# Kernel tuning notes

Hardware: AMD Instinct MI355X
Metric: run time of the kernel (lower is better)

Reference implementation:

```python
import jax, jax.numpy as jnp
import numpy as np

B, S, D, H, F = 16, 512, 768, 12, 3072
E = 4      # unique sequence-level experts
M = 4      # inner SwitchFeedForward experts
SW = 128   # switch encoder dim
EPS = 1e-12


def setup_inputs() -> dict:
    key = jax.random.key(0)
    ks = iter(jax.random.split(key, 64))
    def p(shape):
        return jax.random.normal(next(ks), shape, jnp.float32) * 0.02
    inp = {}
    inp['hidden_states'] = jax.random.normal(next(ks), (B, S, D), jnp.float32)
    inp['attention_mask'] = jnp.zeros((B, S), jnp.float32)
    inp['cluster_list'] = jnp.zeros((B,), jnp.int32)
    # router
    inp['sw_enc_w'] = p((D, SW)); inp['sw_enc_b'] = jnp.zeros((SW,), jnp.float32)
    inp['sw_w'] = p((SW, E));     inp['sw_b'] = jnp.zeros((E,), jnp.float32)
    # common attention
    for n in ('q', 'k', 'v', 'o'):
        inp['ca_w' + n] = p((D, D)); inp['ca_b' + n] = jnp.zeros((D,), jnp.float32)
    # unique attentions (stacked over E experts)
    for n in ('q', 'k', 'v', 'o'):
        inp['ua_w' + n] = p((E, D, D)); inp['ua_b' + n] = jnp.zeros((E, D), jnp.float32)
    # common FFN (plain GELU MLP)
    inp['cf_w1'] = p((D, F)); inp['cf_b1'] = jnp.zeros((F,), jnp.float32)
    inp['cf_w2'] = p((F, D)); inp['cf_b2'] = jnp.zeros((D,), jnp.float32)
    # unique FFNs: each is a top-1 SwitchFeedForward with M inner experts
    inp['uf_sw_w'] = p((E, D, M)); inp['uf_sw_b'] = jnp.zeros((E, M), jnp.float32)
    inp['uf_w1'] = p((E, M, D, F)); inp['uf_b1'] = jnp.zeros((E, M, F), jnp.float32)
    inp['uf_w2'] = p((E, M, F, D)); inp['uf_b2'] = jnp.zeros((E, M, D), jnp.float32)
    # output LayerNorm
    inp['ln_g'] = jnp.ones((D,), jnp.float32); inp['ln_b'] = jnp.zeros((D,), jnp.float32)
    return inp


def _attn(x, mask, wq, bq, wk, bk, wv, bv, wo, bo):
    b, s, d = x.shape
    dh = d // H
    q = (x @ wq + bq).reshape(b, s, H, dh)
    k = (x @ wk + bk).reshape(b, s, H, dh)
    v = (x @ wv + bv).reshape(b, s, H, dh)
    sc = jnp.einsum('bqhd,bkhd->bhqk', q, k) / jnp.sqrt(jnp.float32(dh))
    sc = sc + mask[:, None, None, :]
    pr = jax.nn.softmax(sc, axis=-1)
    o = jnp.einsum('bhqk,bkhd->bqhd', pr, v).reshape(b, s, d)
    return o @ wo + bo


def _switch_ffn(x, sww, swb, w1, b1, w2, b2):
    # top-1 token routing over M inner experts, output scaled by route_prob_max
    rp = jax.nn.softmax(x @ sww + swb, axis=-1)            # [b,s,M]
    gate = jax.nn.one_hot(jnp.argmax(rp, -1), M) * jnp.max(rp, -1, keepdims=True)
    h = jax.nn.gelu(jnp.einsum('bsd,mdf->bsmf', x, w1) + b1, approximate=False)
    y = jnp.einsum('bsmf,mfd->bsmd', h, w2) + b2
    return jnp.einsum('bsm,bsmd->bsd', gate, y)


def _forward(hidden_states, attention_mask, sw_enc_w, sw_enc_b, sw_w, sw_b,
             ca_wq, ca_bq, ca_wk, ca_bk, ca_wv, ca_bv, ca_wo, ca_bo,
             ua_wq, ua_bq, ua_wk, ua_bk, ua_wv, ua_bv, ua_wo, ua_bo,
             cf_w1, cf_b1, cf_w2, cf_b2,
             uf_sw_w, uf_sw_b, uf_w1, uf_b1, uf_w2, uf_b2, ln_g, ln_b):
    # sequence-level router: softmax over pooled hidden states, top-1 expert
    pooled = hidden_states.mean(axis=1)                    # [B,D]
    rp = jax.nn.softmax((pooled @ sw_enc_w + sw_enc_b) @ sw_w + sw_b, axis=-1)
    pm = jnp.max(rp, axis=-1)                              # [B]
    sel = jax.nn.one_hot(jnp.argmax(rp, axis=-1), E)       # [B,E]

    common_attn = _attn(hidden_states, attention_mask,
                        ca_wq, ca_bq, ca_wk, ca_bk, ca_wv, ca_bv, ca_wo, ca_bo)
    unique_attn = jnp.zeros_like(hidden_states)
    for i in range(E):
        oi = _attn(hidden_states, attention_mask,
                   ua_wq[i], ua_bq[i], ua_wk[i], ua_bk[i],
                   ua_wv[i], ua_bv[i], ua_wo[i], ua_bo[i])
        unique_attn = unique_attn + sel[:, i, None, None] * oi
    unique_attn = unique_attn * pm[:, None, None]          # scale by route prob
    att_output = common_attn + unique_attn

    unique_ffn = jnp.zeros_like(hidden_states)
    for i in range(E):
        yi = _switch_ffn(att_output, uf_sw_w[i], uf_sw_b[i],
                         uf_w1[i], uf_b1[i], uf_w2[i], uf_b2[i])
        unique_ffn = unique_ffn + sel[:, i, None, None] * yi
    common_ffn = jax.nn.gelu(att_output @ cf_w1 + cf_b1, approximate=False) @ cf_w2 + cf_b2
    ffn_output = common_ffn + unique_ffn                   # dropout is identity (eval)

    x = att_output + ffn_output
    mu = x.mean(-1, keepdims=True)
    var = jnp.mean((x - mu) ** 2, -1, keepdims=True)
    return (x - mu) / jnp.sqrt(var + EPS) * ln_g + ln_b


def reference(hidden_states, attention_mask, cluster_list, sw_enc_w, sw_enc_b, sw_w, sw_b,
              ca_wq, ca_bq, ca_wk, ca_bk, ca_wv, ca_bv, ca_wo, ca_bo,
              ua_wq, ua_bq, ua_wk, ua_bk, ua_wv, ua_bv, ua_wo, ua_bo,
              cf_w1, cf_b1, cf_w2, cf_b2,
              uf_sw_w, uf_sw_b, uf_w1, uf_b1, uf_w2, uf_b2, ln_g, ln_b):
    # cluster_list is only used in the warm-up branch; warm_up_step=0 -> ignored
    return _forward(hidden_states, attention_mask, sw_enc_w, sw_enc_b, sw_w, sw_b,
                    ca_wq, ca_bq, ca_wk, ca_bk, ca_wv, ca_bv, ca_wo, ca_bo,
                    ua_wq, ua_bq, ua_wk, ua_bk, ua_wv, ua_bv, ua_wo, ua_bo,
                    cf_w1, cf_b1, cf_w2, cf_b2,
                    uf_sw_w, uf_sw_b, uf_w1, uf_b1, uf_w2, uf_b2, ln_g, ln_b)
```

## Files before the change

kernel.cpp:

```cpp
#include <hip/hip_runtime.h>
#include <cstdint>
#include <cstddef>

#define Bq  16
#define Sq  512
#define Dq  768
#define Hq  12
#define DHq 64
#define Fq  3072
#define SWq 128
#define NTq 8192

typedef float        f32x4  __attribute__((ext_vector_type(4)));
typedef float        f32x16 __attribute__((ext_vector_type(16)));
typedef unsigned int u32x4  __attribute__((ext_vector_type(4)));
typedef __bf16       bf16x8 __attribute__((ext_vector_type(8)));
typedef _Float16     f16x8  __attribute__((ext_vector_type(8)));
typedef _Float16     f16x4  __attribute__((ext_vector_type(4)));
typedef _Float16     f16x2  __attribute__((ext_vector_type(2)));
typedef int          i32x2  __attribute__((ext_vector_type(2)));

__device__ __forceinline__ unsigned short f2bf(float f){
  unsigned int u = __builtin_bit_cast(unsigned int, f);
  u = (u + 0x7fffu + ((u >> 16) & 1u)) >> 16;
  return (unsigned short)u;
}
__device__ __forceinline__ unsigned int pk2(float a, float b){
  return (unsigned int)f2bf(a) | ((unsigned int)f2bf(b) << 16);
}
__device__ __forceinline__ i32x2 pl32swap(unsigned int a, unsigned int b){
  return __builtin_amdgcn_permlane32_swap((int)a, (int)b, false, false);
}
__device__ __forceinline__ f16x2 cvt_pk(float a, float b){
  return __builtin_bit_cast(f16x2, __builtin_amdgcn_cvt_pkrtz(a, b));
}

typedef __attribute__((address_space(1))) void vg_t;
typedef __attribute__((address_space(3))) void vl_t;
__device__ __forceinline__ void gl_lds16(const void* g, void* l){
  __builtin_amdgcn_global_load_lds((vg_t*)g, (vl_t*)l, 16, 0, 0);
}

__device__ __forceinline__ void swz2d(int &bx, int &by){
  const int gx = gridDim.x, gy = gridDim.y;
  const int nb = gx * gy;
  const int bid = blockIdx.y * gx + blockIdx.x;
  if (((nb & 7) == 0) && ((gy & 7) == 0)){
    const int chunk = nb >> 3;
    const int lb = (bid & 7) * chunk + (bid >> 3);
    const int bw = gx << 3;
    const int band = lb / bw;
    const int wn = lb - band * bw;
    bx = wn >> 3;
    by = (band << 3) + (wn & 7);
  } else {
    bx = blockIdx.x; by = blockIdx.y;
  }
}

__global__ void pooled_partial_k(const float* __restrict__ x, float* __restrict__ part){
  const int b = blockIdx.x, dc = blockIdx.y, z = blockIdx.z;
  const int d = dc*256 + threadIdx.x;
  const float* p = x + (size_t)b*Sq*Dq + (size_t)z*128*Dq + d;
  float s = 0.f;
  #pragma unroll 4
  for (int i = 0; i < 128; i++) s += p[(size_t)i*Dq];
  part[((size_t)z*Bq + b)*Dq + d] = s;
}

__global__ void router_seq_k(const float* __restrict__ part,
    const float* __restrict__ ew, const float* __restrict__ eb,
    const float* __restrict__ sw, const float* __restrict__ sb,
    int* __restrict__ sel, float* __restrict__ pm)
{
  const int b = blockIdx.x, j = threadIdx.x;
  __shared__ float h[SWq];
  __shared__ float pl[Dq];
  #pragma unroll
  for (int i = 0; i < 6; i++){
    int d = j + i*128;
    float s = part[(size_t)(0*Bq+b)*Dq + d] + part[(size_t)(1*Bq+b)*Dq + d]
            + part[(size_t)(2*Bq+b)*Dq + d] + part[(size_t)(3*Bq+b)*Dq + d];
    pl[d] = s * (1.0f/512.0f);
  }
  __syncthreads();
  float a = eb[j];
  for (int d = 0; d < Dq; d++) a += pl[d] * ew[d*SWq + j];
  h[j] = a;
  __syncthreads();
  if (j == 0){
    float lg[4];
    for (int e = 0; e < 4; e++){
      float t = sb[e];
      for (int k = 0; k < SWq; k++) t += h[k] * sw[k*4 + e];
      lg[e] = t;
    }
    float mx = fmaxf(fmaxf(lg[0],lg[1]), fmaxf(lg[2],lg[3]));
    float p[4], ssum = 0.f;
    for (int e = 0; e < 4; e++){ p[e] = expf(lg[e]-mx); ssum += p[e]; }
    int am = 0; float bv = p[0];
    for (int e = 1; e < 4; e++) if (p[e] > bv){ bv = p[e]; am = e; }
    sel[b] = am; pm[b] = bv/ssum;
  }
}

__global__ void split_f16_k(const float* __restrict__ x, _Float16* __restrict__ hh,
                            _Float16* __restrict__ ll, int n4){
  const int i = blockIdx.x*256 + threadIdx.x;
  if (i >= n4) return;
  f32x4 v = ((const f32x4*)x)[i];
  f16x4 vh, vl;
  #pragma unroll
  for (int j = 0; j < 4; j++){
    float s = v[j] * 1024.0f;
    _Float16 a = (_Float16)s;
    vh[j] = a;
    vl[j] = (_Float16)(s - (float)a);
  }
  ((f16x4*)hh)[i] = vh;
  ((f16x4*)ll)[i] = vl;
}

__global__ void transpose_f16s_k(const float* __restrict__ src,
    _Float16* __restrict__ dH, _Float16* __restrict__ dL,
    int K, int N, long srcStride, long dstStride, int rowOff)
{
  __shared__ float t[64][65];
  const int tid = threadIdx.x;
  const size_t so = (size_t)blockIdx.z * srcStride;
  const size_t dof = (size_t)blockIdx.z * dstStride;
  const int k0 = blockIdx.y * 64, n0 = blockIdx.x * 64;
  const int r = tid >> 2, c0 = (tid & 3) * 16;
  const float* sp = src + so + (size_t)(k0 + r) * N + n0 + c0;
  #pragma unroll
  for (int cc = 0; cc < 16; cc += 4){
    f32x4 v = *(const f32x4*)(sp + cc);
    t[r][c0+cc] = v[0]; t[r][c0+cc+1] = v[1]; t[r][c0+cc+2] = v[2]; t[r][c0+cc+3] = v[3];
  }
  __syncthreads();
  _Float16* ph = dH + dof + (size_t)(rowOff + n0 + r) * K + k0 + c0;
  _Float16* pl = dL + dof + (size_t)(rowOff + n0 + r) * K + k0 + c0;
  #pragma unroll
  for (int cc = 0; cc < 16; cc += 4){
    f16x4 vh, vl;
    #pragma unroll
    for (int j = 0; j < 4; j++){
      float s = t[c0+cc+j][r] * 1024.0f;
      _Float16 a = (_Float16)s;
      vh[j] = a; vl[j] = (_Float16)(s - (float)a);
    }
    *(f16x4*)(ph + cc) = vh;
    *(f16x4*)(pl + cc) = vl;
  }
}

__global__ void concat_bias3_k(const float* __restrict__ bq, const float* __restrict__ bk,
    const float* __restrict__ bv, float* __restrict__ dst, int srcStride)
{
  const int e = blockIdx.y;
  const int i = blockIdx.x*256 + threadIdx.x;
  dst[(size_t)e*2304 + i]        = bq[(size_t)e*srcStride + i];
  dst[(size_t)e*2304 + 768 + i]  = bk[(size_t)e*srcStride + i];
  dst[(size_t)e*2304 + 1536 + i] = bv[(size_t)e*srcStride + i];
}

template<int MT, int BMODE, int OMODE>
__global__ __launch_bounds__(256,2) void gemm_f16s_k(
    const _Float16* __restrict__ AH, const _Float16* __restrict__ AL,
    const _Float16* __restrict__ BH, const _Float16* __restrict__ BL,
    const float* __restrict__ bias, float* __restrict__ C,
    _Float16* __restrict__ Ch, _Float16* __restrict__ Cl,
    int N, int K, long estride, int bias_stride,
    const int* __restrict__ sel, const float* __restrict__ pm)
{
  constexpr int MI = MT / 32;
  constexpr int AI = MT / 64;
  __shared__ _Float16 AsH[MT][32];
  __shared__ _Float16 AsL[MT][32];
  __shared__ _Float16 BsH[128][32];
  __shared__ _Float16 BsL[128][32];
  const int tid = threadIdx.x;
  const int lane = tid & 63, wave = tid >> 6;
  const int wm = wave >> 1, wn = wave & 1;
  int bx, by; swz2d(bx, by);
  const int row0 = by * MT, col0 = bx * 128;
  const _Float16* bh = BH; const _Float16* bl = BL; const float* bp = bias;
  float cs = 1.0f;
  if constexpr (BMODE == 1){
    const int e = sel[row0 >> 9];
    bh += (size_t)e * estride; bl += (size_t)e * estride;
    bp += (size_t)e * bias_stride;
  }
  if constexpr (OMODE == 1) cs = pm[row0 >> 9];

  const int lr = lane >> 2, lk = (lane & 3) * 8;
  const _Float16 *pAH[AI], *pAL[AI], *pBH[2], *pBL[2];
  _Float16 *lAH[AI], *lAL[AI], *lBH[2], *lBL[2];
  #pragma unroll
  for (int j = 0; j < AI; j++){
    const int ia = wave*AI + j;
    pAH[j] = AH + (size_t)(row0 + ia*16 + lr)*K + lk;
    pAL[j] = AL + (size_t)(row0 + ia*16 + lr)*K + lk;
    lAH[j] = &AsH[0][0] + ia*512;
    lAL[j] = &AsL[0][0] + ia*512;
  }
  #pragma unroll
  for (int j = 0; j < 2; j++){
    const int ib = wave*2 + j;
    pBH[j] = bh + (size_t)(col0 + ib*16 + lr)*K + lk;
    pBL[j] = bl + (size_t)(col0 + ib*16 + lr)*K + lk;
    lBH[j] = &BsH[0][0] + ib*512;
    lBL[j] = &BsL[0][0] + ib*512;
  }

  f32x4 acc[MI][4];
  #pragma unroll
  for (int mi=0;mi<MI;mi++)
    #pragma unroll
    for (int ni=0;ni<4;ni++) acc[mi][ni] = (f32x4){0.f,0.f,0.f,0.f};

  for (int k0 = 0; k0 < K; k0 += 32){
    __syncthreads();
    #pragma unroll
    for (int j = 0; j < AI; j++){
      gl_lds16(pAH[j] + k0, lAH[j]);
      gl_lds16(pAL[j] + k0, lAL[j]);
    }
    #pragma unroll
    for (int j = 0; j < 2; j++){
      gl_lds16(pBH[j] + k0, lBH[j]);
      gl_lds16(pBL[j] + k0, lBL[j]);
    }
    __syncthreads();
    f16x8 fah[MI], fal[MI], fbh[4], fbl[4];
    #pragma unroll
    for (int mi=0;mi<MI;mi++){
      const int r = wm*(MT/2) + mi*16 + (lane&15), c = 8*(lane>>4);
      fah[mi] = __builtin_bit_cast(f16x8, *(const u32x4*)&AsH[r][c]);
      fal[mi] = __builtin_bit_cast(f16x8, *(const u32x4*)&AsL[r][c]);
    }
    #pragma unroll
    for (int ni=0;ni<4;ni++){
      const int r = wn*64 + ni*16 + (lane&15), c = 8*(lane>>4);
      fbh[ni] = __builtin_bit_cast(f16x8, *(const u32x4*)&BsH[r][c]);
      fbl[ni] = __builtin_bit_cast(f16x8, *(const u32x4*)&BsL[r][c]);
    }
    #pragma unroll
    for (int mi=0;mi<MI;mi++)
      #pragma unroll
      for (int ni=0;ni<4;ni++){
        acc[mi][ni] = __builtin_amdgcn_mfma_f32_16x16x32_f16(fah[mi], fbh[ni], acc[mi][ni], 0, 0, 0);
        acc[mi][ni] = __builtin_amdgcn_mfma_f32_16x16x32_f16(fah[mi], fbl[ni], acc[mi][ni], 0, 0, 0);
        acc[mi][ni] = __builtin_amdgcn_mfma_f32_16x16x32_f16(fal[mi], fbh[ni], acc[mi][ni], 0, 0, 0);
      }
  }

  const float INV = 1.0f/1048576.0f;
  const int erow = 4*(lane >> 4);
  const int ecol = lane & 15;
  #pragma unroll
  for (int mi=0;mi<MI;mi++)
    #pragma unroll
    for (int ni=0;ni<4;ni++){
      const int c = col0 + wn*64 + ni*16 + ecol;
      const float bb = bp[c];
      #pragma unroll
      for (int r=0;r<4;r++){
        const int R = row0 + wm*(MT/2) + mi*16 + erow + r;
        const float v = acc[mi][ni][r]*INV + bb;
        if constexpr (OMODE == 0){
          C[(size_t)R*N + c] = v;
        } else if constexpr (OMODE == 1){
          C[(size_t)R*N + c] += cs*v;
        } else {
          const float vs = v * 1024.0f;
          const _Float16 hi = (_Float16)vs;
          Ch[(size_t)R*N + c] = hi;
          Cl[(size_t)R*N + c] = (_Float16)(vs - (float)hi);
        }
      }
    }
}

__global__ __launch_bounds__(256,2) void attn_mfma_k(
    const _Float16* __restrict__ qkvH, const _Float16* __restrict__ qkvL,
    const float* __restrict__ mask,
    _Float16* __restrict__ ctxH, _Float16* __restrict__ ctxL)
{
  __shared__ _Float16 Kh[64][72], Kl[64][72];
  __shared__ _Float16 Vh[64][72], Vl[64][72];
  __shared__ float msk[64];
  __shared__ float rsi[4][32];
  const int qb = blockIdx.x, h = blockIdx.y, b = blockIdx.z;
  const int tid = threadIdx.x;
  const int l = tid & 63, w = tid >> 6;
  const int l31 = l & 31, g5 = l >> 5;
  const float SC = 1.0f/8388608.0f;

  u32x4 qfh[4], qfl[4];
  {
    const size_t qoff = (size_t)(b*Sq + qb*128 + w*32 + l31) * 2304 + h*DHq + g5*8;
    #pragma unroll
    for (int c = 0; c < 4; c++){
      qfh[c] = *(const u32x4*)(qkvH + qoff + c*16);
      qfl[c] = *(const u32x4*)(qkvL + qoff + c*16);
    }
  }
  f32x16 oacc[2];
  #pragma unroll
  for (int nt = 0; nt < 2; nt++)
    #pragma unroll
    for (int i = 0; i < 16; i++) oacc[nt][i] = 0.f;
  float rsl = 0.f;
  const float* mrow = mask + b*Sq;

  for (int kt = 0; kt < 8; kt++){
    __syncthreads();
    {
      const size_t krow = (size_t)(b*Sq + kt*64 + l) * 2304 + 768 + h*DHq;
      #pragma unroll
      for (int i = 0; i < 2; i++){
        const int ch = w + i*4;
        *(u32x4*)&Kh[l][ch*8] = *(const u32x4*)(qkvH + krow + ch*8);
        *(u32x4*)&Kl[l][ch*8] = *(const u32x4*)(qkvL + krow + ch*8);
      }
      const size_t vrow = krow + 768 + w*16;
      f16x8 v0 = __builtin_bit_cast(f16x8, *(const u32x4*)(qkvH + vrow));
      f16x8 v1 = __builtin_bit_cast(f16x8, *(const u32x4*)(qkvH + vrow + 8));
      f16x8 u0 = __builtin_bit_cast(f16x8, *(const u32x4*)(qkvL + vrow));
      f16x8 u1 = __builtin_bit_cast(f16x8, *(const u32x4*)(qkvL + vrow + 8));
      #pragma unroll
      for (int i = 0; i < 8; i++){
        Vh[w*16 + i][l] = v0[i]; Vh[w*16 + 8 + i][l] = v1[i];
        Vl[w*16 + i][l] = u0[i]; Vl[w*16 + 8 + i][l] = u1[i];
      }
      if (tid < 64) msk[tid] = mrow[kt*64 + tid] + 6.9314718055994531f;
    }
    __syncthreads();

    f32x16 sacc[2];
    #pragma unroll
    for (int mt = 0; mt < 2; mt++)
      #pragma unroll
      for (int i = 0; i < 16; i++) sacc[mt][i] = 0.f;
    #pragma unroll
    for (int mt = 0; mt < 2; mt++){
      #pragma unroll
      for (int c = 0; c < 4; c++){
        f16x8 kh = __builtin_bit_cast(f16x8, *(const u32x4*)&Kh[mt*32 + l31][c*16 + g5*8]);
        f16x8 kl = __builtin_bit_cast(f16x8, *(const u32x4*)&Kl[mt*32 + l31][c*16 + g5*8]);
        f16x8 qh = __builtin_bit_cast(f16x8, qfh[c]);
        f16x8 ql = __builtin_bit_cast(f16x8, qfl[c]);
        sacc[mt] = __builtin_amdgcn_mfma_f32_32x32x16_f16(kh, qh, sacc[mt], 0, 0, 0);
        sacc[mt] = __builtin_amdgcn_mfma_f32_32x32x16_f16(kh, ql, sacc[mt], 0, 0, 0);
        sacc[mt] = __builtin_amdgcn_mfma_f32_32x32x16_f16(kl, qh, sacc[mt], 0, 0, 0);
      }
    }

    unsigned int hP[2][4][2], lP[2][4][2];
    #pragma unroll
    for (int mt = 0; mt < 2; mt++){
      #pragma unroll
      for (int m = 0; m < 4; m++){
        f32x4 mk = *(const f32x4*)&msk[mt*32 + m*8 + g5*4];
        float p0 = __expf(fmaf(sacc[mt][4*m+0], SC, mk[0]));
        float p1 = __expf(fmaf(sacc[mt][4*m+1], SC, mk[1]));
        float p2 = __expf(fmaf(sacc[mt][4*m+2], SC, mk[2]));
        float p3 = __expf(fmaf(sacc[mt][4*m+3], SC, mk[3]));
        rsl += (p0 + p1) + (p2 + p3);
        f16x2 h0 = cvt_pk(p0, p1);
        f16x2 h1 = cvt_pk(p2, p3);
        f16x2 e0, e1;
        e0[0] = (_Float16)(p0 - (float)h0[0]); e0[1] = (_Float16)(p1 - (float)h0[1]);
        e1[0] = (_Float16)(p2 - (float)h1[0]); e1[1] = (_Float16)(p3 - (float)h1[1]);
        hP[mt][m][0] = __builtin_bit_cast(unsigned int, h0);
        hP[mt][m][1] = __builtin_bit_cast(unsigned int, h1);
        lP[mt][m][0] = __builtin_bit_cast(unsigned int, e0);
        lP[mt][m][1] = __builtin_bit_cast(unsigned int, e1);
      }
    }

    #pragma unroll
    for (int mt = 0; mt < 2; mt++){
      #pragma unroll
      for (int cc = 0; cc < 2; cc++){
        i32x2 sh0 = pl32swap(hP[mt][2*cc][0], hP[mt][2*cc+1][0]);
        i32x2 sh1 = pl32swap(hP[mt][2*cc][1], hP[mt][2*cc+1][1]);
        i32x2 sl0 = pl32swap(lP[mt][2*cc][0], lP[mt][2*cc+1][0]);
        i32x2 sl1 = pl32swap(lP[mt][2*cc][1], lP[mt][2*cc+1][1]);
        u32x4 pah = (u32x4){(unsigned)sh0[0], (unsigned)sh1[0], (unsigned)sh0[1], (unsigned)sh1[1]};
        u32x4 pal = (u32x4){(unsigned)sl0[0], (unsigned)sl1[0], (unsigned)sl0[1], (unsigned)sl1[1]};
        f16x8 ph = __builtin_bit_cast(f16x8, pah);
        f16x8 pe = __builtin_bit_cast(f16x8, pal);
        const int kof = (mt*2 + cc)*16 + g5*8;
        #pragma unroll
        for (int nt = 0; nt < 2; nt++){
          f16x8 vh = __builtin_bit_cast(f16x8, *(const u32x4*)&Vh[nt*32 + l31][kof]);
          f16x8 vl = __builtin_bit_cast(f16x8, *(const u32x4*)&Vl[nt*32 + l31][kof]);
          oacc[nt] = __builtin_amdgcn_mfma_f32_32x32x16_f16(ph, vh, oacc[nt], 0, 0, 0);
          oacc[nt] = __builtin_amdgcn_mfma_f32_32x32x16_f16(ph, vl, oacc[nt], 0, 0, 0);
          oacc[nt] = __builtin_amdgcn_mfma_f32_32x32x16_f16(pe, vh, oacc[nt], 0, 0, 0);
        }
      }
    }
  }

  {
    unsigned int rb = __builtin_bit_cast(unsigned int, rsl);
    i32x2 sw = pl32swap(rb, rb);
    float partner = __builtin_bit_cast(float, (l >= 32) ? sw[0] : sw[1]);
    float tot = rsl + partner;
    if (l < 32) rsi[w][l31] = 1.0f / tot;
  }
  __syncthreads();

  const size_t obase = (size_t)(b*Sq + qb*128 + w*32);
  #pragma unroll
  for (int nt = 0; nt < 2; nt++){
    const int col = h*DHq + nt*32 + l31;
    #pragma unroll
    for (int r = 0; r < 16; r++){
      const int q = (r&3) + 8*(r>>2) + 4*g5;
      const float v = oacc[nt][r] * rsi[w][q];
      const _Float16 hi = (_Float16)v;
      const size_t off = (obase + q)*Dq + col;
      ctxH[off] = hi;
      ctxL[off] = (_Float16)(v - (float)hi);
    }
  }
}

__global__ void transpose_bf16_k(const float* __restrict__ src, unsigned short* __restrict__ dst,
                                 int K, int N)
{
  __shared__ float t[64][65];
  const int tid = threadIdx.x;
  const size_t mo = (size_t)blockIdx.z * K * N;
  const int k0 = blockIdx.y * 64, n0 = blockIdx.x * 64;
  const int r = tid >> 2, c0 = (tid & 3) * 16;
  const float* sp = src + mo + (size_t)(k0 + r) * N + n0 + c0;
  #pragma unroll
  for (int cc = 0; cc < 16; cc += 4){
    f32x4 v = *(const f32x4*)(sp + cc);
    t[r][c0+cc] = v[0]; t[r][c0+cc+1] = v[1]; t[r][c0+cc+2] = v[2]; t[r][c0+cc+3] = v[3];
  }
  __syncthreads();
  unsigned short* dp = dst + mo + (size_t)(n0 + r) * K + k0 + c0;
  u32x4 h0, h1v;
  #pragma unroll
  for (int i = 0; i < 4; i++) h0[i]  = pk2(t[c0+2*i  ][r], t[c0+2*i+1][r]);
  #pragma unroll
  for (int i = 0; i < 4; i++) h1v[i] = pk2(t[c0+8+2*i][r], t[c0+9+2*i][r]);
  *(u32x4*)(dp)     = h0;
  *(u32x4*)(dp + 8) = h1v;
}

template<int MT, int AMODE, int OMODE, bool GELU_, bool GROUPED>
__global__ __launch_bounds__(256,2) void gemm_bf16_k(
    const void* __restrict__ Av, const unsigned short* __restrict__ BT,
    const float* __restrict__ bias, float* __restrict__ Cf, unsigned short* __restrict__ Cb,
    int N, int K,
    const int* __restrict__ tile_g, const int* __restrict__ tile_r0,
    const int* __restrict__ grp_off, const int* __restrict__ n_tiles,
    const int* __restrict__ tok_idx, const float* __restrict__ gate_s,
    size_t bstride, int bias_stride)
{
  constexpr int MI = MT / 32;
  constexpr int AI = MT / 64;
  __shared__ unsigned short As[2][MT][32];
  __shared__ unsigned short Bs[2][128][32];
  const int tid = threadIdx.x;
  const int lane = tid & 63, wave = tid >> 6;
  const int wm = wave >> 1, wn = wave & 1;
  int col0, row0, gend = 1 << 30, g = 0;
  if constexpr (GROUPED){
    const int gx = gridDim.x;
    const int nb = gx * gridDim.y;
    const int bid = blockIdx.y * gx + blockIdx.x;
    int lb = bid;
    if ((nb & 7) == 0) lb = (bid & 7) * (nb >> 3) + (bid >> 3);
    const int t = lb / gx;
    col0 = (lb - t * gx) * 128;
    if (t >= *n_tiles) return;
    g = tile_g[t];
    row0 = grp_off[g] + tile_r0[t];
    gend = grp_off[g+1];
  } else {
    int bx, by; swz2d(bx, by);
    row0 = by * MT;
    col0 = bx * 128;
  }
  const unsigned short* Bp = BT + (size_t)g * bstride;
  const float* bp = bias + (size_t)g * bias_stride;

  const int lr = lane >> 2, lk8 = (lane & 3) * 8;
  const unsigned short* pB[2];
  #pragma unroll
  for (int j = 0; j < 2; j++){
    const int ib = wave*2 + j;
    pB[j] = Bp + (size_t)(col0 + ib*16 + lr)*K + lk8;
  }
  auto stageB = [&](int c, int kk){
    gl_lds16(pB[0] + kk, &Bs[0][0][0] + c*4096 + (wave*2+0)*512);
    gl_lds16(pB[1] + kk, &Bs[0][0][0] + c*4096 + (wave*2+1)*512);
  };
  const unsigned short* pA2[AI];
  const float* afp = nullptr; int sa_r = 0, sa_k = 0;
  if constexpr (AMODE == 2){
    #pragma unroll
    for (int j = 0; j < AI; j++){
      int r = row0 + (wave*AI + j)*16 + lr;
      if constexpr (GROUPED) r = (r < gend - 1) ? r : (gend - 1);
      pA2[j] = (const unsigned short*)Av + (size_t)r*K + lk8;
    }
  } else {
    sa_r = (MT == 128) ? (tid >> 1) : (tid >> 2);
    sa_k = (MT == 128) ? ((tid & 1) * 16) : ((tid & 3) * 8);
    int arow = row0 + sa_r;
    if constexpr (GROUPED) arow = (arow < gend - 1) ? arow : (gend - 1);
    if constexpr (AMODE == 1) arow = tok_idx[arow];
    afp = (const float*)Av + (size_t)arow * K + sa_k;
  }
  auto stageA2 = [&](int c, int kk){
    #pragma unroll
    for (int j = 0; j < AI; j++)
      gl_lds16(pA2[j] + kk, &As[0][0][0] + c*(MT*32) + (wave*AI + j)*512);
  };

  f32x4 acc[MI][4];
  #pragma unroll
  for (int mi=0;mi<MI;mi++)
    #pragma unroll
    for (int ni=0;ni<4;ni++) acc[mi][ni] = (f32x4){0.f,0.f,0.f,0.f};

  const int nt = K >> 5;
  if constexpr (AMODE == 2){
    stageA2(0, 0);
  } else {
    f32x4 f0 = *(const f32x4*)(afp);
    f32x4 f1 = *(const f32x4*)(afp + 4);
    u32x4 al0;
    al0[0]=pk2(f0[0],f0[1]); al0[1]=pk2(f0[2],f0[3]); al0[2]=pk2(f1[0],f1[1]); al0[3]=pk2(f1[2],f1[3]);
    *(u32x4*)&As[0][sa_r][sa_k] = al0;
    if constexpr (MT == 128){
      f32x4 f2 = *(const f32x4*)(afp + 8);
      f32x4 f3 = *(const f32x4*)(afp + 12);
      u32x4 al1;
      al1[0]=pk2(f2[0],f2[1]); al1[1]=pk2(f2[2],f2[3]); al1[2]=pk2(f3[0],f3[1]); al1[3]=pk2(f3[2],f3[3]);
      *(u32x4*)&As[0][sa_r][sa_k + 8] = al1;
    }
  }
  stageB(0, 0);

  int cur = 0;
  for (int t = 0; t < nt; t++){
    __syncthreads();
    const int k1 = (t + 1) << 5;
    f32x4 f0n, f1n, f2n, f3n;
    const bool nxt = (t + 1 < nt);
    if (nxt){
      if constexpr (AMODE == 2){
        stageA2(cur ^ 1, k1);
      } else {
        f0n = *(const f32x4*)(afp + k1);
        f1n = *(const f32x4*)(afp + k1 + 4);
        if constexpr (MT == 128){
          f2n = *(const f32x4*)(afp + k1 + 8);
          f3n = *(const f32x4*)(afp + k1 + 12);
        }
      }
      stageB(cur ^ 1, k1);
    }
    bf16x8 af[MI], bfr[4];
    #pragma unroll
    for (int mi=0;mi<MI;mi++){
      u32x4 tt = *(const u32x4*)&As[cur][wm*(MT/2) + mi*16 + (lane&15)][8*(lane>>4)];
      af[mi] = __builtin_bit_cast(bf16x8, tt);
    }
    #pragma unroll
    for (int ni=0;ni<4;ni++){
      u32x4 tt = *(const u32x4*)&Bs[cur][wn*64 + ni*16 + (lane&15)][8*(lane>>4)];
      bfr[ni] = __builtin_bit_cast(bf16x8, tt);
    }
    #pragma unroll
    for (int mi=0;mi<MI;mi++)
      #pragma unroll
      for (int ni=0;ni<4;ni++)
        acc[mi][ni] = __builtin_amdgcn_mfma_f32_16x16x32_bf16(af[mi], bfr[ni], acc[mi][ni], 0, 0, 0);
    if (nxt){
      if constexpr (AMODE != 2){
        u32x4 al0;
        al0[0]=pk2(f0n[0],f0n[1]); al0[1]=pk2(f0n[2],f0n[3]); al0[2]=pk2(f1n[0],f1n[1]); al0[3]=pk2(f1n[2],f1n[3]);
        *(u32x4*)&As[cur^1][sa_r][sa_k] = al0;
        if constexpr (MT == 128){
          u32x4 al1;
          al1[0]=pk2(f2n[0],f2n[1]); al1[1]=pk2(f2n[2],f2n[3]); al1[2]=pk2(f3n[0],f3n[1]); al1[3]=pk2(f3n[2],f3n[3]);
          *(u32x4*)&As[cur^1][sa_r][sa_k + 8] = al1;
        }
      }
    }
    cur ^= 1;
  }

  const int erow = 4*(lane >> 4);
  const int ecol = lane & 15;
  #pragma unroll
  for (int mi=0;mi<MI;mi++)
    #pragma unroll
    for (int ni=0;ni<4;ni++){
      const int c = col0 + wn*64 + ni*16 + ecol;
      const float bb = bp[c];
      #pragma unroll
      for (int r=0;r<4;r++){
        const int R = row0 + wm*(MT/2) + mi*16 + erow + r;
        if (GROUPED && R >= gend) continue;
        float v = acc[mi][ni][r] + bb;
        if (GELU_) v = 0.5f*v*(1.0f + erff(v*0.70710678118654752f));
        if constexpr (OMODE == 0){
          Cb[(size_t)R*N + c] = f2bf(v);
        } else if constexpr (OMODE == 1){
          Cf[(size_t)R*N + c] = v;
        } else {
          const int tok = tok_idx[R];
          const float gt = gate_s[R];
          float* p = Cf + (size_t)tok*N + c;
          *p += gt*v;
        }
      }
    }
}

__global__ void token_router_k(const float* __restrict__ att, const int* __restrict__ sel,
    const float* __restrict__ sww, const float* __restrict__ swb,
    int* __restrict__ grp, float* __restrict__ gate, int* __restrict__ grp_cnt)
{
  const int t = blockIdx.x*4 + (threadIdx.x >> 6);
  const int lane = threadIdx.x & 63;
  const int e = sel[t >> 9];
  const float* x = att + (size_t)t * Dq;
  const float* w = sww + (size_t)e * Dq * 4;
  float a0=0.f, a1=0.f, a2=0.f, a3=0.f;
  #pragma unroll 4
  for (int i = 0; i < 12; i++){
    const int d = lane + i*64;
    const float xv = x[d];
    f32x4 wv = *(const f32x4*)&w[d*4];
    a0 += xv*wv[0]; a1 += xv*wv[1]; a2 += xv*wv[2]; a3 += xv*wv[3];
  }
  #pragma unroll
  for (int off = 32; off; off >>= 1){
    a0 += __shfl_xor(a0, off); a1 += __shfl_xor(a1, off);
    a2 += __shfl_xor(a2, off); a3 += __shfl_xor(a3, off);
  }
  if (lane == 0){
    const float l0 = a0 + swb[e*4+0], l1 = a1 + swb[e*4+1];
    const float l2 = a2 + swb[e*4+2], l3 = a3 + swb[e*4+3];
    const float mx = fmaxf(fmaxf(l0,l1), fmaxf(l2,l3));
    const float p0 = expf(l0-mx), p1 = expf(l1-mx), p2 = expf(l2-mx), p3 = expf(l3-mx);
    const float ssum = p0+p1+p2+p3;
    int am = 0; float bv = p0;
    if (p1 > bv){ bv=p1; am=1; }
    if (p2 > bv){ bv=p2; am=2; }
    if (p3 > bv){ bv=p3; am=3; }
    grp[t] = e*4 + am;
    gate[t] = bv/ssum;
    atomicAdd(&grp_cnt[e*4 + am], 1);
  }
}

__global__ void build_offsets_k(const int* __restrict__ grp_cnt, int* __restrict__ grp_off,
    int* __restrict__ tg128, int* __restrict__ tr128, int* __restrict__ nt128,
    int* __restrict__ tg64, int* __restrict__ tr64, int* __restrict__ nt64)
{
  int off = 0, n1 = 0, n2 = 0;
  for (int g = 0; g < 16; g++){
    grp_off[g] = off;
    const int c = grp_cnt[g];
    for (int r0 = 0; r0 < c; r0 += 128){ tg128[n1] = g; tr128[n1] = r0; n1++; }
    for (int r0 = 0; r0 < c; r0 += 64){  tg64[n2]  = g; tr64[n2]  = r0; n2++; }
    off += c;
  }
  grp_off[16] = off;
  *nt128 = n1; *nt64 = n2;
}

__global__ void scatter_k(const int* __restrict__ grp, const float* __restrict__ gate,
    const int* __restrict__ grp_off, int* __restrict__ fill,
    int* __restrict__ tok_idx, float* __restrict__ gate_s)
{
  const int t = blockIdx.x*256 + threadIdx.x;
  const int g = grp[t];
  const int pos = grp_off[g] + atomicAdd(&fill[g], 1);
  tok_idx[pos] = t;
  gate_s[pos] = gate[t];
}

__global__ __launch_bounds__(256) void final_ln_k(const float* __restrict__ att,
    const float* __restrict__ acc, const float* __restrict__ lg,
    const float* __restrict__ lb, float* __restrict__ out)
{
  const int row = blockIdx.x, tid = threadIdx.x;
  const float* a = att + (size_t)row * Dq;
  const float* c = acc + (size_t)row * Dq;
  float x[3];
  #pragma unroll
  for (int i = 0; i < 3; i++) x[i] = a[tid + 256*i] + c[tid + 256*i];
  __shared__ float red[256];
  red[tid] = x[0] + x[1] + x[2];
  __syncthreads();
  for (int st = 128; st; st >>= 1){
    if (tid < st) red[tid] += red[tid + st];
    __syncthreads();
  }
  const float mu = red[0] * (1.0f/768.0f);
  __syncthreads();
  const float d0 = x[0]-mu, d1 = x[1]-mu, d2 = x[2]-mu;
  red[tid] = d0*d0 + d1*d1 + d2*d2;
  __syncthreads();
  for (int st = 128; st; st >>= 1){
    if (tid < st) red[tid] += red[tid + st];
    __syncthreads();
  }
  const float inv = 1.0f/sqrtf(red[0]*(1.0f/768.0f) + 1e-12f);
  #pragma unroll
  for (int i = 0; i < 3; i++){
    const int col = tid + 256*i;
    out[(size_t)row*Dq + col] = (x[i]-mu)*inv*lg[col] + lb[col];
  }
}

extern "C" void kernel_launch(void* const* d_in, const int* in_sizes, int n_in,
                              void* d_out, int out_size, void* d_ws, size_t ws_size,
                              hipStream_t stream)
{
  (void)in_sizes; (void)n_in; (void)out_size; (void)ws_size;
  const float* hs    = (const float*)d_in[0];
  const float* amask = (const float*)d_in[1];
  const float* sw_enc_w = (const float*)d_in[3];
  const float* sw_enc_b = (const float*)d_in[4];
  const float* sw_w  = (const float*)d_in[5];
  const float* sw_b  = (const float*)d_in[6];
  const float* ca_wq = (const float*)d_in[7];
  const float* ca_bq = (const float*)d_in[8];
  const float* ca_wk = (const float*)d_in[9];
  const float* ca_bk = (const float*)d_in[10];
  const float* ca_wv = (const float*)d_in[11];
  const float* ca_bv = (const float*)d_in[12];
  const float* ca_wo = (const float*)d_in[13];
  const float* ca_bo = (const float*)d_in[14];
  const float* ua_wq = (const float*)d_in[15];
  const float* ua_bq = (const float*)d_in[16];
  const float* ua_wk = (const float*)d_in[17];
  const float* ua_bk = (const float*)d_in[18];
  const float* ua_wv = (const float*)d_in[19];
  const float* ua_bv = (const float*)d_in[20];
  const float* ua_wo = (const float*)d_in[21];
  const float* ua_bo = (const float*)d_in[22];
  const float* cf_w1 = (const float*)d_in[23];
  const float* cf_b1 = (const float*)d_in[24];
  const float* cf_w2 = (const float*)d_in[25];
  const float* cf_b2 = (const float*)d_in[26];
  const float* uf_sw_w = (const float*)d_in[27];
  const float* uf_sw_b = (const float*)d_in[28];
  const float* uf_w1 = (const float*)d_in[29];
  const float* uf_b1 = (const float*)d_in[30];
  const float* uf_w2 = (const float*)d_in[31];
  const float* uf_b2 = (const float*)d_in[32];
  const float* ln_g  = (const float*)d_in[33];
  const float* ln_b  = (const float*)d_in[34];
  float* out = (float*)d_out;

  char* W = (char*)d_ws;
  int*   sel     = (int*)(W + 0);
  float* pm      = (float*)(W + 64);
  int*   grp_cnt = (int*)(W + 128);
  int*   fill    = (int*)(W + 192);
  int*   ntile   = (int*)(W + 256);
  int*   ntile64 = (int*)(W + 320);
  int*   grp_off = (int*)(W + 512);
  int*   tile_g  = (int*)(W + 1024);
  int*   tile_r  = (int*)(W + 2048);
  int*   tile_g64= (int*)(W + 3072);
  int*   tile_r64= (int*)(W + 4096);

  float* att  = (float*)(W + 8192);
  float* facc = (float*)(W + 25174016);
  const size_t X = 50339840;
  _Float16* hsH  = (_Float16*)(W + X);
  _Float16* hsL  = (_Float16*)(W + X + 12582912);
  _Float16* qkvH = (_Float16*)(W + X + 25165824);
  _Float16* qkvL = (_Float16*)(W + X + 62914560);
  _Float16* ctxH = (_Float16*)(W + X + 100663296);
  _Float16* ctxL = (_Float16*)(W + X + 113246208);
  _Float16* wqkv_cH = (_Float16*)(W + X + 125829120);
  _Float16* wqkv_cL = (_Float16*)(W + X + 129368064);
  _Float16* wqkv_uH = (_Float16*)(W + X + 132907008);
  _Float16* wqkv_uL = (_Float16*)(W + X + 147062784);
  _Float16* wo_cH   = (_Float16*)(W + X + 161218560);
  _Float16* wo_cL   = (_Float16*)(W + X + 162398208);
  _Float16* wo_uH   = (_Float16*)(W + X + 163577856);
  _Float16* wo_uL   = (_Float16*)(W + X + 168296448);
  float* qkvb_c = (float*)(W + X + 173015040);
  float* qkvb_u = (float*)(W + X + 173024256);
  float* partb  = (float*)(W + X + 173061120);

  unsigned short* w1T = (unsigned short*)(W + X);
  unsigned short* w2T = (unsigned short*)(W + X + 80216064);
  unsigned short* h1  = (unsigned short*)(W + X + 160432128);
  int*   grp     = (int*)(W + 261103616);
  float* gate    = (float*)(W + 261136384);
  int*   tok_idx = (int*)(W + 261169152);
  float* gate_s  = (float*)(W + 261201920);

  hipMemsetAsync(W, 0, 512, stream);

  pooled_partial_k<<<dim3(Bq,3,4),256,0,stream>>>(hs, partb);
  router_seq_k<<<Bq,128,0,stream>>>(partb, sw_enc_w, sw_enc_b, sw_w, sw_b, sel, pm);

  split_f16_k<<<6144,256,0,stream>>>(hs, hsH, hsL, NTq*Dq/4);
  transpose_f16s_k<<<dim3(12,12,1),256,0,stream>>>(ca_wq, wqkv_cH, wqkv_cL, Dq, Dq, 0, 0, 0);
  transpose_f16s_k<<<dim3(12,12,1),256,0,stream>>>(ca_wk, wqkv_cH, wqkv_cL, Dq, Dq, 0, 0, 768);
  transpose_f16s_k<<<dim3(12,12,1),256,0,stream>>>(ca_wv, wqkv_cH, wqkv_cL, Dq, Dq, 0, 0, 1536);
  transpose_f16s_k<<<dim3(12,12,4),256,0,stream>>>(ua_wq, wqkv_uH, wqkv_uL, Dq, Dq, (long)Dq*Dq, (long)2304*768, 0);
  transpose_f16s_k<<<dim3(12,12,4),256,0,stream>>>(ua_wk, wqkv_uH, wqkv_uL, Dq, Dq, (long)Dq*Dq, (long)2304*768, 768);
  transpose_f16s_k<<<dim3(12,12,4),256,0,stream>>>(ua_wv, wqkv_uH, wqkv_uL, Dq, Dq, (long)Dq*Dq, (long)2304*768, 1536);
  transpose_f16s_k<<<dim3(12,12,1),256,0,stream>>>(ca_wo, wo_cH, wo_cL, Dq, Dq, 0, 0, 0);
  transpose_f16s_k<<<dim3(12,12,4),256,0,stream>>>(ua_wo, wo_uH, wo_uL, Dq, Dq, (long)Dq*Dq, (long)Dq*Dq, 0);
  concat_bias3_k<<<dim3(3,1),256,0,stream>>>(ca_bq, ca_bk, ca_bv, qkvb_c, 0);
  concat_bias3_k<<<dim3(3,4),256,0,stream>>>(ua_bq, ua_bk, ua_bv, qkvb_u, 768);

  gemm_f16s_k<128,0,2><<<dim3(18,64),256,0,stream>>>(hsH, hsL, wqkv_cH, wqkv_cL, qkvb_c,
      nullptr, qkvH, qkvL, 2304, Dq, 0, 0, nullptr, nullptr);
  attn_mfma_k<<<dim3(4,Hq,Bq),256,0,stream>>>(qkvH, qkvL, amask, ctxH, ctxL);
  gemm_f16s_k<64,0,0><<<dim3(6,128),256,0,stream>>>(ctxH, ctxL, wo_cH, wo_cL, ca_bo,
      att, nullptr, nullptr, Dq, Dq, 0, 0, nullptr, nullptr);

  gemm_f16s_k<128,1,2><<<dim3(18,64),256,0,stream>>>(hsH, hsL, wqkv_uH, wqkv_uL, qkvb_u,
      nullptr, qkvH, qkvL, 2304, Dq, (long)2304*768, 2304, sel, nullptr);
  attn_mfma_k<<<dim3(4,Hq,Bq),256,0,stream>>>(qkvH, qkvL, amask, ctxH, ctxL);
  gemm_f16s_k<64,1,1><<<dim3(6,128),256,0,stream>>>(ctxH, ctxL, wo_uH, wo_uL, ua_bo,
      att, nullptr, nullptr, Dq, Dq, (long)Dq*Dq, Dq, sel, pm);

  transpose_bf16_k<<<dim3(48,12,1), 256,0,stream>>>(cf_w1, w1T, Dq, Fq);
  transpose_bf16_k<<<dim3(48,12,16),256,0,stream>>>(uf_w1, w1T + 2359296, Dq, Fq);
  transpose_bf16_k<<<dim3(12,48,1), 256,0,stream>>>(cf_w2, w2T, Fq, Dq);
  transpose_bf16_k<<<dim3(12,48,16),256,0,stream>>>(uf_w2, w2T + 2359296, Fq, Dq);

  gemm_bf16_k<128,0,0,true,false><<<dim3(24,64),256,0,stream>>>((const void*)att, w1T, cf_b1, nullptr, h1,
      Fq, Dq, nullptr,nullptr,nullptr,nullptr,nullptr,nullptr, (size_t)0, 0);
  gemm_bf16_k<64,2,1,false,false><<<dim3(6,128),256,0,stream>>>((const void*)h1, w2T, cf_b2, facc, nullptr,
      Dq, Fq, nullptr,nullptr,nullptr,nullptr,nullptr,nullptr, (size_t)0, 0);

  token_router_k<<<2048,256,0,stream>>>(att, sel, uf_sw_w, uf_sw_b, grp, gate, grp_cnt);
  build_offsets_k<<<1,1,0,stream>>>(grp_cnt, grp_off, tile_g, tile_r, ntile, tile_g64, tile_r64, ntile64);
  scatter_k<<<32,256,0,stream>>>(grp, gate, grp_off, fill, tok_idx, gate_s);

  gemm_bf16_k<128,1,0,true,true><<<dim3(24,80),256,0,stream>>>((const void*)att, w1T + 2359296, uf_b1, nullptr, h1,
      Fq, Dq, tile_g, tile_r, grp_off, ntile, tok_idx, gate_s, (size_t)2359296, Fq);
  gemm_bf16_k<64,2,2,false,true><<<dim3(6,144),256,0,stream>>>((const void*)h1, w2T + 2359296, uf_b2, facc, nullptr,
      Dq, Fq, tile_g64, tile_r64, grp_off, ntile64, tok_idx, gate_s, (size_t)2359296, Dq);

  final_ln_k<<<NTq,256,0,stream>>>(att, facc, ln_g, ln_b, out);
}
```

Baseline: 1.148 ms.

## Emit bf16 copy of attention output in epilogue and accumulate FFN into att

The attention output-projection GEMMs now also write a bf16 copy of the attention output, so the FFN GEMMs load A through direct global-to-LDS async copies instead of converting fp32 to bf16 in registers. The FFN down-projections accumulate straight into the attention buffer, which removes the separate facc buffer and one read in the final LayerNorm. Token routing is moved earlier, before the transposes, but still reads fp32 att before the common FFN adds into it. The cost is an extra bf16 write in the attention epilogue, and the OMODE 1 path becomes a read-modify-write, so results depend on kernel ordering.

Measured after the change: 1.133 ms. About the same (-1.4%).

```diff
diff --git a/kernel.cpp b/kernel.cpp
--- a/kernel.cpp
+++ b/kernel.cpp
@@ -170,6 +170,7 @@
     const _Float16* __restrict__ BH, const _Float16* __restrict__ BL,
     const float* __restrict__ bias, float* __restrict__ C,
     _Float16* __restrict__ Ch, _Float16* __restrict__ Cl,
+    unsigned short* __restrict__ Cb16,
     int N, int K, long estride, int bias_stride,
     const int* __restrict__ sel, const float* __restrict__ pm)
 {
@@ -270,8 +271,11 @@
         const float v = acc[mi][ni][r]*INV + bb;
         if constexpr (OMODE == 0){
           C[(size_t)R*N + c] = v;
+          Cb16[(size_t)R*N + c] = f2bf(v);
         } else if constexpr (OMODE == 1){
-          C[(size_t)R*N + c] += cs*v;
+          const float val = C[(size_t)R*N + c] + cs*v;
+          C[(size_t)R*N + c] = val;
+          Cb16[(size_t)R*N + c] = f2bf(val);
         } else {
           const float vs = v * 1024.0f;
           const _Float16 hi = (_Float16)vs;
@@ -455,9 +459,9 @@
   *(u32x4*)(dp + 8) = h1v;
 }
 
-template<int MT, int AMODE, int OMODE, bool GELU_, bool GROUPED>
+template<int MT, bool GATHER, int OMODE, bool GELU_, bool GROUPED>
 __global__ __launch_bounds__(256,2) void gemm_bf16_k(
-    const void* __restrict__ Av, const unsigned short* __restrict__ BT,
+    const unsigned short* __restrict__ A, const unsigned short* __restrict__ BT,
     const float* __restrict__ bias, float* __restrict__ Cf, unsigned short* __restrict__ Cb,
     int N, int K,
     const int* __restrict__ tile_g, const int* __restrict__ tile_r0,
@@ -504,27 +508,18 @@
     gl_lds16(pB[0] + kk, &Bs[0][0][0] + c*4096 + (wave*2+0)*512);
     gl_lds16(pB[1] + kk, &Bs[0][0][0] + c*4096 + (wave*2+1)*512);
   };
-  const unsigned short* pA2[AI];
-  const float* afp = nullptr; int sa_r = 0, sa_k = 0;
-  if constexpr (AMODE == 2){
-    #pragma unroll
-    for (int j = 0; j < AI; j++){
-      int r = row0 + (wave*AI + j)*16 + lr;
-      if constexpr (GROUPED) r = (r < gend - 1) ? r : (gend - 1);
-      pA2[j] = (const unsigned short*)Av + (size_t)r*K + lk8;
-    }
-  } else {
-    sa_r = (MT == 128) ? (tid >> 1) : (tid >> 2);
-    sa_k = (MT == 128) ? ((tid & 1) * 16) : ((tid & 3) * 8);
-    int arow = row0 + sa_r;
-    if constexpr (GROUPED) arow = (arow < gend - 1) ? arow : (gend - 1);
-    if constexpr (AMODE == 1) arow = tok_idx[arow];
-    afp = (const float*)Av + (size_t)arow * K + sa_k;
-  }
-  auto stageA2 = [&](int c, int kk){
+  const unsigned short* pA[AI];
+  #pragma unroll
+  for (int j = 0; j < AI; j++){
+    int r = row0 + (wave*AI + j)*16 + lr;
+    if constexpr (GROUPED) r = (r < gend - 1) ? r : (gend - 1);
+    if constexpr (GATHER) r = tok_idx[r];
+    pA[j] = A + (size_t)r*K + lk8;
+  }
+  auto stageA = [&](int c, int kk){
     #pragma unroll
     for (int j = 0; j < AI; j++)
-      gl_lds16(pA2[j] + kk, &As[0][0][0] + c*(MT*32) + (wave*AI + j)*512);
+      gl_lds16(pA[j] + kk, &As[0][0][0] + c*(MT*32) + (wave*AI + j)*512);
   };
 
   f32x4 acc[MI][4];
@@ -534,41 +529,15 @@
     for (int ni=0;ni<4;ni++) acc[mi][ni] = (f32x4){0.f,0.f,0.f,0.f};
 
   const int nt = K >> 5;
-  if constexpr (AMODE == 2){
-    stageA2(0, 0);
-  } else {
-    f32x4 f0 = *(const f32x4*)(afp);
-    f32x4 f1 = *(const f32x4*)(afp + 4);
-    u32x4 al0;
-    al0[0]=pk2(f0[0],f0[1]); al0[1]=pk2(f0[2],f0[3]); al0[2]=pk2(f1[0],f1[1]); al0[3]=pk2(f1[2],f1[3]);
-    *(u32x4*)&As[0][sa_r][sa_k] = al0;
-    if constexpr (MT == 128){
-      f32x4 f2 = *(const f32x4*)(afp + 8);
-      f32x4 f3 = *(const f32x4*)(afp + 12);
-      u32x4 al1;
-      al1[0]=pk2(f2[0],f2[1]); al1[1]=pk2(f2[2],f2[3]); al1[2]=pk2(f3[0],f3[1]); al1[3]=pk2(f3[2],f3[3]);
-      *(u32x4*)&As[0][sa_r][sa_k + 8] = al1;
-    }
-  }
+  stageA(0, 0);
   stageB(0, 0);
 
   int cur = 0;
   for (int t = 0; t < nt; t++){
     __syncthreads();
     const int k1 = (t + 1) << 5;
-    f32x4 f0n, f1n, f2n, f3n;
-    const bool nxt = (t + 1 < nt);
-    if (nxt){
-      if constexpr (AMODE == 2){
-        stageA2(cur ^ 1, k1);
-      } else {
-        f0n = *(const f32x4*)(afp + k1);
-        f1n = *(const f32x4*)(afp + k1 + 4);
-        if constexpr (MT == 128){
-          f2n = *(const f32x4*)(afp + k1 + 8);
-          f3n = *(const f32x4*)(afp + k1 + 12);
-        }
-      }
+    if (t + 1 < nt){
+      stageA(cur ^ 1, k1);
       stageB(cur ^ 1, k1);
     }
     bf16x8 af[MI], bfr[4];
@@ -587,18 +556,6 @@
       #pragma unroll
       for (int ni=0;ni<4;ni++)
         acc[mi][ni] = __builtin_amdgcn_mfma_f32_16x16x32_bf16(af[mi], bfr[ni], acc[mi][ni], 0, 0, 0);
-    if (nxt){
-      if constexpr (AMODE != 2){
-        u32x4 al0;
-        al0[0]=pk2(f0n[0],f0n[1]); al0[1]=pk2(f0n[2],f0n[3]); al0[2]=pk2(f1n[0],f1n[1]); al0[3]=pk2(f1n[2],f1n[3]);
-        *(u32x4*)&As[cur^1][sa_r][sa_k] = al0;
-        if constexpr (MT == 128){
-          u32x4 al1;
-          al1[0]=pk2(f2n[0],f2n[1]); al1[1]=pk2(f2n[2],f2n[3]); al1[2]=pk2(f3n[0],f3n[1]); al1[3]=pk2(f3n[2],f3n[3]);
-          *(u32x4*)&As[cur^1][sa_r][sa_k + 8] = al1;
-        }
-      }
-    }
     cur ^= 1;
   }
 
@@ -619,7 +576,7 @@
         if constexpr (OMODE == 0){
           Cb[(size_t)R*N + c] = f2bf(v);
         } else if constexpr (OMODE == 1){
-          Cf[(size_t)R*N + c] = v;
+          Cf[(size_t)R*N + c] += v;
         } else {
           const int tok = tok_idx[R];
           const float gt = gate_s[R];
@@ -696,15 +653,13 @@
 }
 
 __global__ __launch_bounds__(256) void final_ln_k(const float* __restrict__ att,
-    const float* __restrict__ acc, const float* __restrict__ lg,
-    const float* __restrict__ lb, float* __restrict__ out)
+    const float* __restrict__ lg, const float* __restrict__ lb, float* __restrict__ out)
 {
   const int row = blockIdx.x, tid = threadIdx.x;
   const float* a = att + (size_t)row * Dq;
-  const float* c = acc + (size_t)row * Dq;
   float x[3];
   #pragma unroll
-  for (int i = 0; i < 3; i++) x[i] = a[tid + 256*i] + c[tid + 256*i];
+  for (int i = 0; i < 3; i++) x[i] = a[tid + 256*i];
   __shared__ float red[256];
   red[tid] = x[0] + x[1] + x[2];
   __syncthreads();
@@ -783,8 +738,8 @@
   int*   tile_g64= (int*)(W + 3072);
   int*   tile_r64= (int*)(W + 4096);
 
-  float* att  = (float*)(W + 8192);
-  float* facc = (float*)(W + 25174016);
+  float* att = (float*)(W + 8192);
+  unsigned short* attb = (unsigned short*)(W + 25174016);
   const size_t X = 50339840;
   _Float16* hsH  = (_Float16*)(W + X);
   _Float16* hsL  = (_Float16*)(W + X + 12582912);
@@ -830,35 +785,35 @@
   concat_bias3_k<<<dim3(3,4),256,0,stream>>>(ua_bq, ua_bk, ua_bv, qkvb_u, 768);
 
   gemm_f16s_k<128,0,2><<<dim3(18,64),256,0,stream>>>(hsH, hsL, wqkv_cH, wqkv_cL, qkvb_c,
-      nullptr, qkvH, qkvL, 2304, Dq, 0, 0, nullptr, nullptr);
+      nullptr, qkvH, qkvL, nullptr, 2304, Dq, 0, 0, nullptr, nullptr);
   attn_mfma_k<<<dim3(4,Hq,Bq),256,0,stream>>>(qkvH, qkvL, amask, ctxH, ctxL);
   gemm_f16s_k<64,0,0><<<dim3(6,128),256,0,stream>>>(ctxH, ctxL, wo_cH, wo_cL, ca_bo,
-      att, nullptr, nullptr, Dq, Dq, 0, 0, nullptr, nullptr);
+      att, nullptr, nullptr, attb, Dq, Dq, 0, 0, nullptr, nullptr);
 
   gemm_f16s_k<128,1,2><<<dim3(18,64),256,0,stream>>>(hsH, hsL, wqkv_uH, wqkv_uL, qkvb_u,
-      nullptr, qkvH, qkvL, 2304, Dq, (long)2304*768, 2304, sel, nullptr);
+      nullptr, qkvH, qkvL, nullptr, 2304, Dq, (long)2304*768, 2304, sel, nullptr);
   attn_mfma_k<<<dim3(4,Hq,Bq),256,0,stream>>>(qkvH, qkvL, amask, ctxH, ctxL);
   gemm_f16s_k<64,1,1><<<dim3(6,128),256,0,stream>>>(ctxH, ctxL, wo_uH, wo_uL, ua_bo,
-      att, nullptr, nullptr, Dq, Dq, (long)Dq*Dq, Dq, sel, pm);
+      att, nullptr, nullptr, attb, Dq, Dq, (long)Dq*Dq, Dq, sel, pm);
+
+  token_router_k<<<2048,256,0,stream>>>(att, sel, uf_sw_w, uf_sw_b, grp, gate, grp_cnt);
+  build_offsets_k<<<1,1,0,stream>>>(grp_cnt, grp_off, tile_g, tile_r, ntile, tile_g64, tile_r64, ntile64);
+  scatter_k<<<32,256,0,stream>>>(grp, gate, grp_off, fill, tok_idx, gate_s);
 
   transpose_bf16_k<<<dim3(48,12,1), 256,0,stream>>>(cf_w1, w1T, Dq, Fq);
   transpose_bf16_k<<<dim3(48,12,16),256,0,stream>>>(uf_w1, w1T + 2359296, Dq, Fq);
   transpose_bf16_k<<<dim3(12,48,1), 256,0,stream>>>(cf_w2, w2T, Fq, Dq);
   transpose_bf16_k<<<dim3(12,48,16),256,0,stream>>>(uf_w2, w2T + 2359296, Fq, Dq);
 
-  gemm_bf16_k<128,0,0,true,false><<<dim3(24,64),256,0,stream>>>((const void*)att, w1T, cf_b1, nullptr, h1,
+  gemm_bf16_k<128,false,0,true,false><<<dim3(24,64),256,0,stream>>>(attb, w1T, cf_b1, nullptr, h1,
       Fq, Dq, nullptr,nullptr,nullptr,nullptr,nullptr,nullptr, (size_t)0, 0);
-  gemm_bf16_k<64,2,1,false,false><<<dim3(6,128),256,0,stream>>>((const void*)h1, w2T, cf_b2, facc, nullptr,
+  gemm_bf16_k<64,false,1,false,false><<<dim3(6,128),256,0,stream>>>(h1, w2T, cf_b2, att, nullptr,
       Dq, Fq, nullptr,nullptr,nullptr,nullptr,nullptr,nullptr, (size_t)0, 0);
 
-  token_router_k<<<2048,256,0,stream>>>(att, sel, uf_sw_w, uf_sw_b, grp, gate, grp_cnt);
-  build_offsets_k<<<1,1,0,stream>>>(grp_cnt, grp_off, tile_g, tile_r, ntile, tile_g64, tile_r64, ntile64);
-  scatter_k<<<32,256,0,stream>>>(grp, gate, grp_off, fill, tok_idx, gate_s);
-
-  gemm_bf16_k<128,1,0,true,true><<<dim3(24,80),256,0,stream>>>((const void*)att, w1T + 2359296, uf_b1, nullptr, h1,
+  gemm_bf16_k<128,true,0,true,true><<<dim3(24,80),256,0,stream>>>(attb, w1T + 2359296, uf_b1, nullptr, h1,
       Fq, Dq, tile_g, tile_r, grp_off, ntile, tok_idx, gate_s, (size_t)2359296, Fq);
-  gemm_bf16_k<64,2,2,false,true><<<dim3(6,144),256,0,stream>>>((const void*)h1, w2T + 2359296, uf_b2, facc, nullptr,
+  gemm_bf16_k<64,false,2,false,true><<<dim3(6,144),256,0,stream>>>(h1, w2T + 2359296, uf_b2, att, nullptr,
       Dq, Fq, tile_g64, tile_r64, grp_off, ntile64, tok_idx, gate_s, (size_t)2359296, Dq);
 
-  final_ln_k<<<NTq,256,0,stream>>>(att, facc, ln_g, ln_b, out);
-}
+  final_ln_k<<<NTq,256,0,stream>>>(att, ln_g, ln_b, out);
+}
```
